# Performance work log

Measured on AMD Instinct MI355X. Metric: run time of the kernel, lower is better.

## Reference

```python
import jax, jax.numpy as jnp
import numpy as np

H = W = 512
A = 256  # number of projection angles


def setup_inputs() -> dict:
    key = jax.random.key(0)
    k1, k2 = jax.random.split(key)
    data = jax.random.normal(k1, (1, 1, H, W), dtype=jnp.float32)
    # angles uniform in [0, pi) -- realistic tomographic scan range
    angles = jax.random.uniform(k2, (A,), dtype=jnp.float32) * np.float32(np.pi)
    return {"data": data, "angles": angles}


def _radon(data, angles):
    B, C, h, w = data.shape  # B == C == 1 structurally required by the torch module
    nA = angles.shape[0]
    cos = jnp.cos(angles)
    sin = jnp.sin(angles)

    # F.affine_grid(align_corners=False) base coordinates: pixel centers in [-1, 1]
    xs = (2.0 * jnp.arange(w, dtype=data.dtype) + 1.0) / w - 1.0  # [W]
    ys = (2.0 * jnp.arange(h, dtype=data.dtype) + 1.0) / h - 1.0  # [H]
    by, bx = jnp.meshgrid(ys, xs, indexing="ij")  # [H,W]

    # theta built from -angles: rows [cos a, sin a, 0; -sin a, cos a, 0]
    gx = cos[:, None, None] * bx + sin[:, None, None] * by  # [A,H,W]
    gy = -sin[:, None, None] * bx + cos[:, None, None] * by  # [A,H,W]

    # grid_sample(align_corners=False): unnormalize to input pixel coords
    ix = ((gx + 1.0) * w - 1.0) * 0.5
    iy = ((gy + 1.0) * h - 1.0) * 0.5

    x0 = jnp.floor(ix).astype(jnp.int32)
    y0 = jnp.floor(iy).astype(jnp.int32)
    x1 = x0 + 1
    y1 = y0 + 1
    wx1 = ix - x0.astype(data.dtype)
    wx0 = 1.0 - wx1
    wy1 = iy - y0.astype(data.dtype)
    wy0 = 1.0 - wy1

    img = data[0, 0]  # [H,W]

    def gather(yy, xx):
        # zero padding: out-of-range taps contribute 0
        valid = (xx >= 0) & (xx < w) & (yy >= 0) & (yy < h)
        v = img[jnp.clip(yy, 0, h - 1), jnp.clip(xx, 0, w - 1)]
        return jnp.where(valid, v, jnp.zeros((), data.dtype))

    rotated = (wy0 * (wx0 * gather(y0, x0) + wx1 * gather(y0, x1))
               + wy1 * (wx0 * gather(y1, x0) + wx1 * gather(y1, x1)))  # [A,H,W]

    proj = jnp.sum(rotated, axis=1)  # sum over height -> [A,W]
    return proj.reshape(1, 1, nA, w)


def reference(data, angles):
    return _radon(data, angles)
```

## Files before the change

### kernel.cpp

```cpp
#include <hip/hip_runtime.h>


#define HH 512
#define WW 512
#define NA 256
#define XC 64
#define YC 64
#define NXC 8
#define NYC 8
#define NW 8
#define RM 96
#define SM 97
#define PAD 112
#define PW (WW + 2 * PAD)
#define PH (HH + 2 * PAD)

typedef __fp16 h2 __attribute__((ext_vector_type(2)));

#if __has_builtin(__builtin_amdgcn_fdot2)
#define FDOT2(a, b, cc) __builtin_amdgcn_fdot2((a), (b), (cc), false)
#else
static __device__ __forceinline__ float FDOT2(h2 a, h2 b, float cc) {
    return fmaf((float)a.x, (float)b.x, fmaf((float)a.y, (float)b.y, cc));
}
#endif

static __device__ __forceinline__ unsigned pack_pair(float v0, float v1) {
    h2 p = __builtin_amdgcn_cvt_pkrtz(v0, v1);
    return __builtin_bit_cast(unsigned, p);
}

__global__ __launch_bounds__(256) void padpack_kernel(
    const float* __restrict__ img, unsigned* __restrict__ Pv)
{
    const int c = blockIdx.x * 256 + threadIdx.x;
    const int r = blockIdx.y;
    if (c >= PW) return;
    const int gr = r - PAD, gc = c - PAD;
    float v0 = 0.0f, v1 = 0.0f;
    if ((unsigned)gc < (unsigned)WW) {
        if ((unsigned)gr       < (unsigned)HH) v0 = img[gr * WW + gc];
        if ((unsigned)(gr + 1) < (unsigned)HH) v1 = img[(gr + 1) * WW + gc];
    }
    Pv[r * PW + c] = pack_pair(v0, v1);
}

template <int S, bool PADDED>
__device__ __forceinline__ float radon_chunks(
    const void* __restrict__ srcv, unsigned* __restrict__ tile,
    const float s, const float c, const int lane, const int wid, const int x0)
{
    const float u  = (float)(x0 + lane) + (0.5f - 256.0f);
    const float u0 = (float)x0 + (0.5f - 256.0f);
    const float u1 = u0 + 63.0f;

    const float cu0 = c * u0, cu1 = c * u1;
    const float cumin = fminf(cu0, cu1), cumax = fmaxf(cu0, cu1);
    const float su0 = -s * u0, su1 = -s * u1;
    const float sumin = fminf(su0, su1), sumax = fmaxf(su0, su1);

    const float bcc = fmaf(c, u, 255.5f);
    const float brc = fmaf(-s, u, 255.5f);

    const unsigned* __restrict__ Porg =
        (const unsigned*)srcv + (PADDED ? (PAD * PW + PAD) : 0);

    float acc = 0.0f;

    for (int yc = 0; yc < NYC; ++yc) {
        const float v0 = (float)(yc * YC) + (0.5f - 256.0f);
        const float v1 = v0 + 63.0f;

        const float sv0 = s * v0, sv1 = s * v1;
        const float cv0 = c * v0, cv1 = c * v1;
        const float cvmin = fminf(cv0, cv1), cvmax = fmaxf(cv0, cv1);

        const float cx_min = cumin + sv0 + 255.5f;
        const float cx_max = cumax + sv1 + 255.5f;
        const float rx_min = sumin + cvmin + 255.5f;
        const float rx_max = sumax + cvmax + 255.5f;

        const int c_lo = (int)floorf(cx_min);
        const int c_hi = (int)floorf(cx_max) + 1;
        const int r_lo = (int)floorf(rx_min);
        const int r_hi = (int)floorf(rx_max) + 1;

        if (c_lo > WW - 1 || c_hi < 0 || r_lo > HH - 1 || r_hi < 0) continue;

        __syncthreads();

        if (PADDED) {
            if (lane < 23) {
                const unsigned* g = Porg + (r_lo + wid) * PW + c_lo + lane * 4;
                int loff = wid * S;
#pragma unroll
                for (int k = 0; k < 12; ++k) {
                    __builtin_amdgcn_global_load_lds(
                        (const __attribute__((address_space(1))) void*)g,
                        (__attribute__((address_space(3))) void*)&tile[loff],
                        16, 0, 0);
                    g += NW * PW;
                    loff += NW * S;
                }
            }
        } else {
            const float* __restrict__ img = (const float*)srcv;
            for (int r = wid; r < RM; r += NW) {
                const int gr = r_lo + r;
                for (int cc = lane; cc < 92; cc += 64) {
                    const int gc = c_lo + cc;
                    float a0 = 0.0f, a1 = 0.0f;
                    if ((unsigned)gc < (unsigned)WW) {
                        if ((unsigned)gr       < (unsigned)HH) a0 = img[gr * WW + gc];
                        if ((unsigned)(gr + 1) < (unsigned)HH) a1 = img[(gr + 1) * WW + gc];
                    }
                    tile[r * S + cc] = pack_pair(a0, a1);
                }
            }
        }

        __syncthreads();

        const float bc = bcc - (float)c_lo;
        const float br = brc - (float)r_lo;
        const float vyb = v0 + (float)(wid * 8);
        const float cx0 = fmaf(s, vyb, bc);
        const float rx0 = fmaf(c, vyb, br);

#pragma unroll
        for (int i = 0; i < 8; ++i) {
            const float cxl = fmaf(s, (float)i, cx0);
            const float rxl = fmaf(c, (float)i, rx0);
            const int ci = (int)cxl;
            const int ri = (int)rxl;
            const float wx1 = __builtin_amdgcn_fractf(cxl);
            const float wy1 = __builtin_amdgcn_fractf(rxl);
            const float wx0 = 1.0f - wx1;
            const float wy0 = 1.0f - wy1;
            const h2 wy = __builtin_amdgcn_cvt_pkrtz(wy0, wy1);

            __builtin_assume(ri >= 0 && ri < RM - 1);
            __builtin_assume(ci >= 0 && ci < 92);
            const int ad = ri * S + ci;

            const unsigned w0 = tile[ad];
            const unsigned w1 = tile[ad + 1];

            const float left  = FDOT2(__builtin_bit_cast(h2, w0), wy, 0.0f);
            const float right = FDOT2(__builtin_bit_cast(h2, w1), wy, 0.0f);
            acc = fmaf(wx0, left, acc);
            acc = fmaf(wx1, right, acc);
        }
    }

    return acc;
}

template <bool PADDED>
__global__ __launch_bounds__(512, 8) void radon_kernel(
    const void* __restrict__ src,
    const float* __restrict__ angles, float* __restrict__ out)
{
    __shared__ unsigned tile[RM * SM];
    __shared__ float red[512];

    const int tid  = threadIdx.x;
    const int lane = tid & 63;
    const int wid  = tid >> 6;

    const int a  = blockIdx.x >> 3;
    const int x0 = (blockIdx.x & 7) * XC;

    float s, c;
    sincosf(angles[a], &s, &c);

    float acc;
    if (c >= 0.0f)
        acc = radon_chunks<95, PADDED>(src, tile, s, c, lane, wid, x0);
    else
        acc = radon_chunks<97, PADDED>(src, tile, s, c, lane, wid, x0);

    __syncthreads();
    red[tid] = acc;
    __syncthreads();
    if (tid < 64) {
        float r = red[tid];
#pragma unroll
        for (int k = 1; k < NW; ++k) r += red[k * 64 + tid];
        out[a * WW + x0 + tid] = r;
    }
}

extern "C" void kernel_launch(void* const* d_in, const int* in_sizes, int n_in,
                              void* d_out, int out_size, void* d_ws, size_t ws_size,
                              hipStream_t stream) {
    const float* img    = (const float*)d_in[0];
    const float* angles = (const float*)d_in[1];
    float* out   = (float*)d_out;
    unsigned* Pv = (unsigned*)d_ws;

    const bool padded = (ws_size >= (size_t)PW * PH * sizeof(unsigned));

    if (padded) {
        padpack_kernel<<<dim3((PW + 255) / 256, PH), 256, 0, stream>>>(img, Pv);
        radon_kernel<true><<<dim3(NA * NXC), 512, 0, stream>>>((const void*)Pv, angles, out);
    } else {
        radon_kernel<false><<<dim3(NA * NXC), 512, 0, stream>>>((const void*)img, angles, out);
    }
}
```

Before: 114.3 us.

## Double-buffer LDS tiles with async global-to-LDS prefetch, split kernels by stride

The LDS tile is now double-buffered. The next y-chunk's bounding box is computed and its global_load_lds prefetch issued before the current chunk is consumed, using vmcnt waits and raw barriers to overlap load latency with the bilinear FDOT2 work. The stride specialization is moved to two separate kernel launches that exit early for angles of the other cos sign, and tile origins are clamped to the padded region. LDS use doubles and the occupancy hint drops from 8 to 4 blocks. The second launch adds overhead because half of each grid's blocks exit immediately.

```diff
diff --git a/kernel.cpp b/kernel.cpp
--- a/kernel.cpp
+++ b/kernel.cpp
@@ -45,11 +45,54 @@
     Pv[r * PW + c] = pack_pair(v0, v1);
 }
 
-template <int S, bool PADDED>
-__device__ __forceinline__ float radon_chunks(
-    const void* __restrict__ srcv, unsigned* __restrict__ tile,
-    const float s, const float c, const int lane, const int wid, const int x0)
+__global__ __launch_bounds__(512) void radon_fallback(
+    const float* __restrict__ img, const float* __restrict__ angles,
+    float* __restrict__ out)
 {
+    const int x = threadIdx.x, a = blockIdx.x;
+    float s, c;
+    sincosf(angles[a], &s, &c);
+    const float u = (float)x + (0.5f - 256.0f);
+    const float cu = fmaf(c, u, 255.5f), cv = fmaf(-s, u, 255.5f);
+    float acc = 0.0f;
+    for (int y = 0; y < HH; ++y) {
+        const float vy = (float)y + (0.5f - 256.0f);
+        const float ix = fmaf(s, vy, cu), iy = fmaf(c, vy, cv);
+        const float fx = floorf(ix), fy = floorf(iy);
+        const int xi = (int)fx, yi = (int)fy;
+        const float wx1 = ix - fx, wy1 = iy - fy;
+        const float mx0 = ((unsigned)xi       < (unsigned)WW) ? 1.0f - wx1 : 0.0f;
+        const float mx1 = ((unsigned)(xi + 1) < (unsigned)WW) ? wx1 : 0.0f;
+        const float my0 = ((unsigned)yi       < (unsigned)HH) ? 1.0f - wy1 : 0.0f;
+        const float my1 = ((unsigned)(yi + 1) < (unsigned)HH) ? wy1 : 0.0f;
+        const int x0 = min(max(xi, 0), WW - 1), x1 = min(max(xi + 1, 0), WW - 1);
+        const int y0 = min(max(yi, 0), HH - 1), y1 = min(max(yi + 1, 0), HH - 1);
+        acc = fmaf(my0, fmaf(mx1, img[y0 * WW + x1], mx0 * img[y0 * WW + x0]), acc);
+        acc = fmaf(my1, fmaf(mx1, img[y1 * WW + x1], mx0 * img[y1 * WW + x0]), acc);
+    }
+    out[a * WW + x] = acc;
+}
+
+template <int S>
+__global__ __launch_bounds__(512, 4) void radon_kernel(
+    const unsigned* __restrict__ Pv, const float* __restrict__ angles,
+    float* __restrict__ out)
+{
+    __shared__ unsigned tileA[RM * SM];
+    __shared__ unsigned tileB[RM * SM];
+    __shared__ float red[512];
+
+    const int tid  = threadIdx.x;
+    const int lane = tid & 63;
+    const int wid  = tid >> 6;
+
+    const int a  = blockIdx.x >> 3;
+    const int x0 = (blockIdx.x & 7) * XC;
+
+    float s, c;
+    sincosf(angles[a], &s, &c);
+    if ((S == 95) != (c >= 0.0f)) return;
+
     const float u  = (float)(x0 + lane) + (0.5f - 256.0f);
     const float u0 = (float)x0 + (0.5f - 256.0f);
     const float u1 = u0 + 63.0f;
@@ -62,123 +105,91 @@
     const float bcc = fmaf(c, u, 255.5f);
     const float brc = fmaf(-s, u, 255.5f);
 
-    const unsigned* __restrict__ Porg =
-        (const unsigned*)srcv + (PADDED ? (PAD * PW + PAD) : 0);
-
-    float acc = 0.0f;
-
-    for (int yc = 0; yc < NYC; ++yc) {
+    const unsigned* __restrict__ Porg = Pv + PAD * PW + PAD;
+
+    auto bbox = [&](int yc, int& clo, int& rlo, bool& outside) {
         const float v0 = (float)(yc * YC) + (0.5f - 256.0f);
         const float v1 = v0 + 63.0f;
-
         const float sv0 = s * v0, sv1 = s * v1;
         const float cv0 = c * v0, cv1 = c * v1;
         const float cvmin = fminf(cv0, cv1), cvmax = fmaxf(cv0, cv1);
-
-        const float cx_min = cumin + sv0 + 255.5f;
-        const float cx_max = cumax + sv1 + 255.5f;
-        const float rx_min = sumin + cvmin + 255.5f;
-        const float rx_max = sumax + cvmax + 255.5f;
-
-        const int c_lo = (int)floorf(cx_min);
-        const int c_hi = (int)floorf(cx_max) + 1;
-        const int r_lo = (int)floorf(rx_min);
-        const int r_hi = (int)floorf(rx_max) + 1;
-
-        if (c_lo > WW - 1 || c_hi < 0 || r_lo > HH - 1 || r_hi < 0) continue;
-
-        __syncthreads();
-
-        if (PADDED) {
-            if (lane < 23) {
-                const unsigned* g = Porg + (r_lo + wid) * PW + c_lo + lane * 4;
-                int loff = wid * S;
+        const int c_lo = (int)floorf(cumin + sv0 + 255.5f);
+        const int c_hi = (int)floorf(cumax + sv1 + 255.5f) + 1;
+        const int r_lo = (int)floorf(sumin + cvmin + 255.5f);
+        const int r_hi = (int)floorf(sumax + cvmax + 255.5f) + 1;
+        outside = (c_lo > WW - 1) | (c_hi < 0) | (r_lo > HH - 1) | (r_hi < 0);
+        clo = min(max(c_lo, -PAD), WW + PAD - 96);
+        rlo = min(max(r_lo, -PAD), HH + PAD - 96);
+    };
+
+    auto stage = [&](unsigned* dst, int clo, int rlo) {
+        if (lane < 23) {
+            const unsigned* g = Porg + (rlo + wid) * PW + clo + lane * 4;
+            int loff = wid * S;
 #pragma unroll
-                for (int k = 0; k < 12; ++k) {
-                    __builtin_amdgcn_global_load_lds(
-                        (const __attribute__((address_space(1))) void*)g,
-                        (__attribute__((address_space(3))) void*)&tile[loff],
-                        16, 0, 0);
-                    g += NW * PW;
-                    loff += NW * S;
-                }
-            }
-        } else {
-            const float* __restrict__ img = (const float*)srcv;
-            for (int r = wid; r < RM; r += NW) {
-                const int gr = r_lo + r;
-                for (int cc = lane; cc < 92; cc += 64) {
-                    const int gc = c_lo + cc;
-                    float a0 = 0.0f, a1 = 0.0f;
-                    if ((unsigned)gc < (unsigned)WW) {
-                        if ((unsigned)gr       < (unsigned)HH) a0 = img[gr * WW + gc];
-                        if ((unsigned)(gr + 1) < (unsigned)HH) a1 = img[(gr + 1) * WW + gc];
-                    }
-                    tile[r * S + cc] = pack_pair(a0, a1);
-                }
+            for (int k = 0; k < 12; ++k) {
+                __builtin_amdgcn_global_load_lds(
+                    (const __attribute__((address_space(1))) void*)g,
+                    (__attribute__((address_space(3))) void*)&dst[loff],
+                    16, 0, 0);
+                g += NW * PW;
+                loff += NW * S;
             }
         }
-
-        __syncthreads();
-
-        const float bc = bcc - (float)c_lo;
-        const float br = brc - (float)r_lo;
-        const float vyb = v0 + (float)(wid * 8);
-        const float cx0 = fmaf(s, vyb, bc);
-        const float rx0 = fmaf(c, vyb, br);
-
+    };
+
+    float acc = 0.0f;
+
+    int clo_cur, rlo_cur; bool out_cur;
+    bbox(0, clo_cur, rlo_cur, out_cur);
+    stage(tileA, clo_cur, rlo_cur);
+
+    for (int k = 0; k < NYC; ++k) {
+        int clo_nxt = 0, rlo_nxt = 0; bool out_nxt = false;
+        if (k + 1 < NYC) {
+            bbox(k + 1, clo_nxt, rlo_nxt, out_nxt);
+            stage((k + 1) & 1 ? tileB : tileA, clo_nxt, rlo_nxt);
+            asm volatile("s_waitcnt vmcnt(12)" ::: "memory");
+        } else {
+            asm volatile("s_waitcnt vmcnt(0)" ::: "memory");
+        }
+        __builtin_amdgcn_s_barrier();
+
+        if (!out_cur) {
+            const unsigned* __restrict__ tile = (k & 1) ? tileB : tileA;
+            const float bc = bcc - (float)clo_cur;
+            const float br = brc - (float)rlo_cur;
+            const float vyb = (float)(k * YC) + (0.5f - 256.0f) + (float)(wid * 8);
+            const float cx0 = fmaf(s, vyb, bc);
+            const float rx0 = fmaf(c, vyb, br);
 #pragma unroll
-        for (int i = 0; i < 8; ++i) {
-            const float cxl = fmaf(s, (float)i, cx0);
-            const float rxl = fmaf(c, (float)i, rx0);
-            const int ci = (int)cxl;
-            const int ri = (int)rxl;
-            const float wx1 = __builtin_amdgcn_fractf(cxl);
-            const float wy1 = __builtin_amdgcn_fractf(rxl);
-            const float wx0 = 1.0f - wx1;
-            const float wy0 = 1.0f - wy1;
-            const h2 wy = __builtin_amdgcn_cvt_pkrtz(wy0, wy1);
-
-            __builtin_assume(ri >= 0 && ri < RM - 1);
-            __builtin_assume(ci >= 0 && ci < 92);
-            const int ad = ri * S + ci;
-
-            const unsigned w0 = tile[ad];
-            const unsigned w1 = tile[ad + 1];
-
-            const float left  = FDOT2(__builtin_bit_cast(h2, w0), wy, 0.0f);
-            const float right = FDOT2(__builtin_bit_cast(h2, w1), wy, 0.0f);
-            acc = fmaf(wx0, left, acc);
-            acc = fmaf(wx1, right, acc);
+            for (int i = 0; i < 8; ++i) {
+                const float cxl = fmaf(s, (float)i, cx0);
+                const float rxl = fmaf(c, (float)i, rx0);
+                const int ci = (int)cxl;
+                const int ri = (int)rxl;
+                const float wx1 = __builtin_amdgcn_fractf(cxl);
+                const float wy1 = __builtin_amdgcn_fractf(rxl);
+                const float wx0 = 1.0f - wx1;
+                const float wy0 = 1.0f - wy1;
+                const h2 wy = __builtin_amdgcn_cvt_pkrtz(wy0, wy1);
+
+                __builtin_assume(ri >= 0 && ri < RM - 1);
+                __builtin_assume(ci >= 0 && ci < 92);
+                const int ad = ri * S + ci;
+
+                const unsigned w0 = tile[ad];
+                const unsigned w1 = tile[ad + 1];
+                const float left  = FDOT2(__builtin_bit_cast(h2, w0), wy, 0.0f);
+                const float right = FDOT2(__builtin_bit_cast(h2, w1), wy, 0.0f);
+                acc = fmaf(wx0, left, acc);
+                acc = fmaf(wx1, right, acc);
+            }
         }
-    }
-
-    return acc;
-}
-
-template <bool PADDED>
-__global__ __launch_bounds__(512, 8) void radon_kernel(
-    const void* __restrict__ src,
-    const float* __restrict__ angles, float* __restrict__ out)
-{
-    __shared__ unsigned tile[RM * SM];
-    __shared__ float red[512];
-
-    const int tid  = threadIdx.x;
-    const int lane = tid & 63;
-    const int wid  = tid >> 6;
-
-    const int a  = blockIdx.x >> 3;
-    const int x0 = (blockIdx.x & 7) * XC;
-
-    float s, c;
-    sincosf(angles[a], &s, &c);
-
-    float acc;
-    if (c >= 0.0f)
-        acc = radon_chunks<95, PADDED>(src, tile, s, c, lane, wid, x0);
-    else
-        acc = radon_chunks<97, PADDED>(src, tile, s, c, lane, wid, x0);
+        __builtin_amdgcn_s_barrier();
+
+        clo_cur = clo_nxt; rlo_cur = rlo_nxt; out_cur = out_nxt;
+    }
 
     __syncthreads();
     red[tid] = acc;
@@ -199,12 +210,11 @@
     float* out   = (float*)d_out;
     unsigned* Pv = (unsigned*)d_ws;
 
-    const bool padded = (ws_size >= (size_t)PW * PH * sizeof(unsigned));
-
-    if (padded) {
+    if (ws_size >= (size_t)PW * PH * sizeof(unsigned)) {
         padpack_kernel<<<dim3((PW + 255) / 256, PH), 256, 0, stream>>>(img, Pv);
-        radon_kernel<true><<<dim3(NA * NXC), 512, 0, stream>>>((const void*)Pv, angles, out);
+        radon_kernel<95><<<dim3(NA * NXC), 512, 0, stream>>>(Pv, angles, out);
+        radon_kernel<97><<<dim3(NA * NXC), 512, 0, stream>>>(Pv, angles, out);
     } else {
-        radon_kernel<false><<<dim3(NA * NXC), 512, 0, stream>>>((const void*)img, angles, out);
-    }
-}
+        radon_fallback<<<dim3(NA), 512, 0, stream>>>(img, angles, out);
+    }
+}
```

Result: slower. 153.0 us (+33.8%).
